# Performance work log

Measured on AMD Instinct MI355X. Metric: run time of the kernel, lower is better.

Reference implementation:

```python
import jax, jax.numpy as jnp
import numpy as np

N_GRAPHS = 50
EPS = 1e-5
N_NODES, N_EDGES, F, L, N_HEADS = 50000, 800000, 64, 3, 3


def _bn(x, gamma, beta):
    # BatchNorm1d over nodes, training-mode (biased batch statistics)
    m = x.mean(axis=0)
    v = jnp.mean((x - m) ** 2, axis=0)
    return gamma * (x - m) * jax.lax.rsqrt(v + EPS) + beta


def _pna_layer(x, src, dst, preW, preb, postW, postb, linW, linb, avg_log, avg_lin):
    N = x.shape[0]
    # pre-MLP on concatenated (target x_i, source x_j): [E, 2F] -> [E, F]
    h = jnp.concatenate([x[dst], x[src]], axis=-1) @ preW + preb
    ones = jnp.ones((h.shape[0],), h.dtype)
    cnt = jax.ops.segment_sum(ones, dst, num_segments=N)[:, None]
    has = cnt > 0
    deg = jnp.maximum(cnt, 1.0)  # PNAConv clamps degree to >= 1
    mean = jax.ops.segment_sum(h, dst, num_segments=N) / deg
    mean2 = jax.ops.segment_sum(h * h, dst, num_segments=N) / deg
    std = jnp.sqrt(jax.nn.relu(mean2 - mean * mean) + EPS)
    mn = jnp.where(has, jax.ops.segment_min(h, dst, num_segments=N), 0.0)
    mx = jnp.where(has, jax.ops.segment_max(h, dst, num_segments=N), 0.0)
    aggr = jnp.concatenate([mean, mn, mx, std], axis=-1)  # [N, 4F]
    log_deg = jnp.log(deg + 1.0)
    out = jnp.concatenate([aggr,
                           aggr * (log_deg / avg_log),   # amplification
                           aggr * (avg_log / log_deg),   # attenuation
                           aggr * (deg / avg_lin)],      # linear
                          axis=-1)                       # [N, 16F]
    out = jnp.concatenate([x, out], axis=-1) @ postW + postb  # post-MLP [N, F]
    return out @ linW + linb


def _forward(x, deg_hist, preW, preb, postW, postb, linW, linb, bn_g, bn_b,
             sharedW, sharedb, hW1, hb1, hW2, hb2, hW3, hb3, src, dst, batch):
    bins = jnp.arange(deg_hist.shape[0], dtype=deg_hist.dtype)
    tot = deg_hist.sum()
    avg_lin = (bins * deg_hist).sum() / tot
    avg_log = (jnp.log(bins + 1.0) * deg_hist).sum() / tot
    for l in range(preW.shape[0]):  # only num_conv_layers convs run (zip truncation)
        x = _pna_layer(x, src, dst, preW[l], preb[l], postW[l], postb[l],
                       linW[l], linb[l], avg_log, avg_lin)
        x = jax.nn.relu(_bn(x, bn_g[l], bn_b[l]))
    gcnt = jax.ops.segment_sum(jnp.ones((x.shape[0],), x.dtype), batch,
                               num_segments=N_GRAPHS)[:, None]
    g = jax.ops.segment_sum(x, batch, num_segments=N_GRAPHS) / jnp.maximum(gcnt, 1.0)
    g = jax.nn.relu(g @ sharedW + sharedb)  # shared MLP (num_shared=1)
    h1 = jax.nn.relu(jnp.einsum('gd,hdk->hgk', g, hW1) + hb1[:, None, :])
    h2 = jax.nn.relu(jnp.einsum('hgk,hkm->hgm', h1, hW2) + hb2[:, None, :])
    o = jnp.einsum('hgm,hmo->hgo', h2, hW3) + hb3[:, None, :]  # [H, G, 1]
    return jnp.transpose(o[..., 0])  # [G, H] == torch.cat(head outputs, dim=1)


def setup_inputs():
    key = jax.random.key(0)
    ks = jax.random.split(key, 12)

    def w(k, shape, fan_in):
        return jax.random.normal(k, shape, jnp.float32) / np.sqrt(fan_in)

    return {
        "x": jax.random.normal(ks[0], (N_NODES, F), jnp.float32),
        "edge_index": jax.random.randint(ks[1], (2, N_EDGES), 0, N_NODES),
        "batch": jnp.sort(jax.random.randint(ks[2], (N_NODES,), 0, N_GRAPHS)),
        "deg_hist": jax.random.uniform(ks[3], (33,), jnp.float32) + 0.01,
        "preW": w(ks[4], (L, 2 * F, F), 2 * F),
        "preb": jnp.zeros((L, F), jnp.float32),
        "postW": w(ks[5], (L, 17 * F, F), 17 * F),
        "postb": jnp.zeros((L, F), jnp.float32),
        "linW": w(ks[6], (L, F, F), F),
        "linb": jnp.zeros((L, F), jnp.float32),
        "bn_g": jnp.ones((L, F), jnp.float32),
        "bn_b": jnp.zeros((L, F), jnp.float32),
        "sharedW": w(ks[7], (F, F), F),
        "sharedb": jnp.zeros((F,), jnp.float32),
        "hW1": w(ks[8], (N_HEADS, F, 50), F),
        "hb1": jnp.zeros((N_HEADS, 50), jnp.float32),
        "hW2": w(ks[9], (N_HEADS, 50, 25), 50),
        "hb2": jnp.zeros((N_HEADS, 25), jnp.float32),
        "hW3": w(ks[10], (N_HEADS, 25, 1), 25),
        "hb3": jnp.zeros((N_HEADS, 1), jnp.float32),
    }


def reference(x, edge_index, batch, deg_hist, preW, preb, postW, postb,
              linW, linb, bn_g, bn_b, sharedW, sharedb,
              hW1, hb1, hW2, hb2, hW3, hb3):
    return _forward(x, deg_hist, preW, preb, postW, postb, linW, linb,
                    bn_g, bn_b, sharedW, sharedb, hW1, hb1, hW2, hb2,
                    hW3, hb3, edge_index[0], edge_index[1], batch)
```

## Files before the change

kernel.cpp:

```cpp
#include <hip/hip_runtime.h>
#include <math.h>

#define N_NODES 50000
#define N_EDGES 800000
#define NGRAPHS 50
#define NHEADS 3
#define EPS 1e-5f
#define NWIN 196
#define WSH 8

typedef _Float16 half8 __attribute__((ext_vector_type(8)));
typedef _Float16 half2v __attribute__((ext_vector_type(2)));
typedef float f32x4 __attribute__((ext_vector_type(4)));

__global__ void __launch_bounds__(256) k_zero_setup(int* cnt, float* gsum, float* gcnt,
                                                    float* part, float* partq,
                                                    const float* dh, int nbins, float* scal) {
  int gid = blockIdx.x * 256 + threadIdx.x;
  int gs = gridDim.x * 256;
  for (int i = gid; i < N_NODES; i += gs) cnt[i] = 0;
  for (int i = gid; i < NGRAPHS * 64; i += gs) gsum[i] = 0.f;
  for (int i = gid; i < NGRAPHS; i += gs) gcnt[i] = 0.f;
  for (int i = gid; i < 128 * 64; i += gs) { part[i] = 0.f; partq[i] = 0.f; }
  if (blockIdx.x == 0 && threadIdx.x < 64) {
    int t = threadIdx.x;
    float v = (t < nbins) ? dh[t] : 0.f;
    float lv = logf((float)t + 1.f) * v;
    float bv = (float)t * v;
    for (int d = 32; d > 0; d >>= 1) {
      v  += __shfl_down(v,  d, 64);
      lv += __shfl_down(lv, d, 64);
      bv += __shfl_down(bv, d, 64);
    }
    if (t == 0) { scal[0] = lv / v; scal[1] = bv / v; }
  }
}

__global__ void __launch_bounds__(256) k_hist(const int* __restrict__ dst, int* __restrict__ cnt) {
  int e = blockIdx.x * 256 + threadIdx.x;
  if (e < N_EDGES) atomicAdd(&cnt[dst[e]], 1);
}

__global__ void __launch_bounds__(256) k_scan_a(const int* __restrict__ cnt, int* __restrict__ off,
                                                int* __restrict__ blksum) {
  __shared__ int lds[256];
  int t = threadIdx.x;
  int base = blockIdx.x * 1024 + t * 4;
  int v0 = (base + 0 < N_NODES) ? cnt[base + 0] : 0;
  int v1 = (base + 1 < N_NODES) ? cnt[base + 1] : 0;
  int v2 = (base + 2 < N_NODES) ? cnt[base + 2] : 0;
  int v3 = (base + 3 < N_NODES) ? cnt[base + 3] : 0;
  int tsum = v0 + v1 + v2 + v3;
  lds[t] = tsum; __syncthreads();
  for (int d = 1; d < 256; d <<= 1) {
    int x = (t >= d) ? lds[t - d] : 0;
    __syncthreads();
    lds[t] += x;
    __syncthreads();
  }
  int run = lds[t] - tsum;
  if (base + 0 < N_NODES) off[base + 0] = run; run += v0;
  if (base + 1 < N_NODES) off[base + 1] = run; run += v1;
  if (base + 2 < N_NODES) off[base + 2] = run; run += v2;
  if (base + 3 < N_NODES) off[base + 3] = run;
  if (t == 255) blksum[blockIdx.x] = lds[255];
}

__global__ void __launch_bounds__(64) k_scan_b(const int* __restrict__ blksum, int* __restrict__ blkoff) {
  int t = threadIdx.x;
  int own = (t < 49) ? blksum[t] : 0;
  int v = own;
  for (int d = 1; d < 64; d <<= 1) {
    int u = __shfl_up(v, d, 64);
    if (t >= d) v += u;
  }
  if (t < 49) blkoff[t] = v - own;
}

__global__ void __launch_bounds__(256) k_scan_c(int* __restrict__ off, const int* __restrict__ blkoff,
                                                int* __restrict__ wincur) {
  int i = blockIdx.x * 256 + threadIdx.x;
  if (i < N_NODES) {
    int fo = off[i] + blkoff[i >> 10];
    off[i] = fo;
    if ((i & 255) == 0) wincur[i >> WSH] = fo;
  }
  if (i == 0) off[N_NODES] = N_EDGES;
}

__global__ void __launch_bounds__(256) k_part1(const int* __restrict__ src, const int* __restrict__ dst,
                                               int* __restrict__ wincur, int* __restrict__ pairS,
                                               unsigned char* __restrict__ pairDL) {
  __shared__ int hist[256];
  __shared__ int scan[256];
  __shared__ int baseg[256];
  __shared__ int place[256];
  __shared__ int sS[2048];
  __shared__ unsigned char sDL[2048];
  __shared__ unsigned char sW[2048];
  int t = threadIdx.x;
  int base = blockIdx.x * 2048;
  hist[t] = 0;
  __syncthreads();
  int d[8], s[8];
  #pragma unroll
  for (int i = 0; i < 8; ++i) {
    int e = base + t + 256 * i;
    bool val = e < N_EDGES;
    d[i] = val ? dst[e] : -1;
    s[i] = val ? src[e] : 0;
    if (val) atomicAdd(&hist[d[i] >> WSH], 1);
  }
  __syncthreads();
  int v = hist[t];
  scan[t] = v; __syncthreads();
  for (int dd = 1; dd < 256; dd <<= 1) {
    int x = (t >= dd) ? scan[t - dd] : 0;
    __syncthreads();
    scan[t] += x;
    __syncthreads();
  }
  place[t] = scan[t] - v;
  if (v > 0) baseg[t] = atomicAdd(&wincur[t], v);
  __syncthreads();
  #pragma unroll
  for (int i = 0; i < 8; ++i) {
    if (d[i] >= 0) {
      int w = d[i] >> WSH;
      int p = atomicAdd(&place[w], 1);
      sS[p] = s[i] << 6;
      sDL[p] = (unsigned char)(d[i] & 255);
      sW[p] = (unsigned char)w;
    }
  }
  __syncthreads();
  int tot = min(N_EDGES - base, 2048);
  for (int i = t; i < tot; i += 256) {
    int w = sW[i];
    int gidx = baseg[w] + (i - (scan[w] - hist[w]));
    pairS[gidx] = sS[i];
    pairDL[gidx] = sDL[i];
  }
}

__global__ void __launch_bounds__(256) k_part2(const int* __restrict__ off, const int* __restrict__ pairS,
                                               const unsigned char* __restrict__ pairDL,
                                               int* __restrict__ esrc) {
  __shared__ int curW[256];
  __shared__ int offW[257];
  __shared__ int esrcW[6144];
  int w = blockIdx.x, t = threadIdx.x;
  int n0 = w << WSH;
  offW[t] = off[min(n0 + t, N_NODES)];
  if (t == 0) offW[256] = off[min(n0 + 256, N_NODES)];
  curW[t] = 0;
  __syncthreads();
  int start = offW[0];
  int end = offW[256];
  int cnt = end - start;
  if (cnt <= 6144) {
    for (int i = t; i < cnt; i += 256) {
      int s = pairS[start + i];
      int dl = pairDL[start + i];
      int pos = offW[dl] - start + atomicAdd(&curW[dl], 1);
      esrcW[pos] = s;
    }
    __syncthreads();
    for (int i = t; i < cnt; i += 256) esrc[start + i] = esrcW[i];
  } else {
    for (int i = t; i < cnt; i += 256) {
      int s = pairS[start + i];
      int dl = pairDL[start + i];
      int pos = offW[dl] + atomicAdd(&curW[dl], 1);
      esrc[pos] = s;
    }
  }
}

__global__ void __launch_bounds__(256) k_prep(const float* __restrict__ xin, _Float16* __restrict__ xout,
                                              const float* __restrict__ preW, const float* __restrict__ postW,
                                              const float* __restrict__ linW, _Float16* __restrict__ preP,
                                              _Float16* __restrict__ postAP, _Float16* __restrict__ postBP,
                                              _Float16* __restrict__ linP) {
  int t0 = blockIdx.x * 256 + threadIdx.x;
  if (t0 < 400000) {
    const float* s = xin + (size_t)t0 * 8;
    float4 v0 = *(const float4*)s;
    float4 v1 = *(const float4*)(s + 4);
    half8 h = {(_Float16)v0.x, (_Float16)v0.y, (_Float16)v0.z, (_Float16)v0.w,
               (_Float16)v1.x, (_Float16)v1.y, (_Float16)v1.z, (_Float16)v1.w};
    *(half8*)(xout + (size_t)t0 * 8) = h;
    return;
  }
  int t = t0 - 400000;
  if (t < 24576) {
    int l = t >> 13, r = t & 8191;
    int j = r & 7, lane = (r >> 3) & 63, ctg = (r >> 9) & 7, kc = r >> 12;
    int k = kc * 32 + ((lane >> 4) << 3) + j;
    int col = ctg * 16 + (lane & 15);
    const float* W = preW + (size_t)l * 8192;
    float v = (col < 64) ? W[k * 64 + col] : W[(64 + k) * 64 + (col - 64)];
    preP[(size_t)l * 8192 + r] = (_Float16)v;
  } else if (t < 221184) {
    int q = t - 24576;
    int l = q >> 16, r = q & 65535;
    int j = r & 7, lane = (r >> 3) & 63, ct = (r >> 9) & 3, s = (r >> 11) & 3, kc = r >> 13;
    int kp = kc * 32 + ((lane >> 4) << 3) + j;
    int half = kp >> 7, sec = (kp >> 5) & 3, f = kp & 31;
    int korig = sec * 64 + half * 32 + f;
    int col = ct * 16 + (lane & 15);
    postAP[(size_t)l * 65536 + r] = (_Float16)postW[(size_t)l * 69632 + (size_t)(64 + s * 256 + korig) * 64 + col];
  } else if (t < 233472) {
    int q = t - 221184;
    int l = q >> 12, r = q & 4095;
    int j = r & 7, lane = (r >> 3) & 63, ct = (r >> 9) & 3, kc = r >> 11;
    int k = kc * 32 + ((lane >> 4) << 3) + j;
    int col = ct * 16 + (lane & 15);
    postBP[(size_t)l * 4096 + r] = (_Float16)postW[(size_t)l * 69632 + (size_t)k * 64 + col];
  } else if (t < 245760) {
    int q = t - 233472;
    int l = q >> 12, r = q & 4095;
    int j = r & 7, lane = (r >> 3) & 63, ct = (r >> 9) & 3, kc = r >> 11;
    int k = kc * 32 + ((lane >> 4) << 3) + j;
    int col = ct * 16 + (lane & 15);
    linP[(size_t)l * 4096 + r] = (_Float16)linW[(size_t)l * 4096 + (size_t)k * 64 + col];
  }
}

__global__ void __launch_bounds__(256) k_mfma_g1(const _Float16* __restrict__ yin, const float* __restrict__ bnsc,
                                                 const float* __restrict__ bnsh, int applyBN,
                                                 const _Float16* __restrict__ wp, const float* __restrict__ bias,
                                                 _Float16* __restrict__ Aout, _Float16* __restrict__ B0,
                                                 _Float16* __restrict__ B1, _Float16* __restrict__ xout) {
  int t = threadIdx.x, lane = t & 63, wave = t >> 6;
  int r0 = blockIdx.x * 64;
  int mrow = lane & 15, q8 = ((lane >> 4) << 3);
  f32x4 acc[4][2];
  #pragma unroll
  for (int rt = 0; rt < 4; ++rt) { acc[rt][0] = (f32x4)0.f; acc[rt][1] = (f32x4)0.f; }
  #pragma unroll
  for (int kc = 0; kc < 2; ++kc) {
    int k0 = kc * 32 + q8;
    half8 a[4];
    #pragma unroll
    for (int rt = 0; rt < 4; ++rt) {
      int r = min(r0 + rt * 16 + mrow, N_NODES - 1);
      a[rt] = *(const half8*)(yin + (size_t)r * 64 + k0);
    }
    if (applyBN) {
      float4 sc0 = *(const float4*)(bnsc + k0);
      float4 sc1 = *(const float4*)(bnsc + k0 + 4);
      float4 sh0 = *(const float4*)(bnsh + k0);
      float4 sh1 = *(const float4*)(bnsh + k0 + 4);
      #pragma unroll
      for (int rt = 0; rt < 4; ++rt) {
        half8 v = a[rt];
        v[0] = (_Float16)fmaxf((float)v[0] * sc0.x + sh0.x, 0.f);
        v[1] = (_Float16)fmaxf((float)v[1] * sc0.y + sh0.y, 0.f);
        v[2] = (_Float16)fmaxf((float)v[2] * sc0.z + sh0.z, 0.f);
        v[3] = (_Float16)fmaxf((float)v[3] * sc0.w + sh0.w, 0.f);
        v[4] = (_Float16)fmaxf((float)v[4] * sc1.x + sh1.x, 0.f);
        v[5] = (_Float16)fmaxf((float)v[5] * sc1.y + sh1.y, 0.f);
        v[6] = (_Float16)fmaxf((float)v[6] * sc1.z + sh1.z, 0.f);
        v[7] = (_Float16)fmaxf((float)v[7] * sc1.w + sh1.w, 0.f);
        a[rt] = v;
      }
      if (wave == 0) {
        #pragma unroll
        for (int rt = 0; rt < 4; ++rt) {
          int r = min(r0 + rt * 16 + mrow, N_NODES - 1);
          *(half8*)(xout + (size_t)r * 64 + k0) = a[rt];
        }
      }
    }
    #pragma unroll
    for (int ci = 0; ci < 2; ++ci) {
      int ctg = wave * 2 + ci;
      half8 b = *(const half8*)(wp + (size_t)((kc * 8 + ctg) * 64 + lane) * 8);
      #pragma unroll
      for (int rt = 0; rt < 4; ++rt)
        acc[rt][ci] = __builtin_amdgcn_mfma_f32_16x16x32_f16(a[rt], b, acc[rt][ci], 0, 0, 0);
    }
  }
  #pragma unroll
  for (int ci = 0; ci < 2; ++ci) {
    int col = (wave * 2 + ci) * 16 + mrow;
    float bv = (col < 64) ? bias[col] : 0.f;
    _Float16* outp;
    int stride;
    if (col < 64)      { outp = Aout + col;       stride = 64; }
    else if (col < 96) { outp = B0 + (col - 64);  stride = 32; }
    else               { outp = B1 + (col - 96);  stride = 32; }
    #pragma unroll
    for (int rt = 0; rt < 4; ++rt)
      #pragma unroll
      for (int reg = 0; reg < 4; ++reg) {
        int row = r0 + rt * 16 + ((lane >> 4) << 2) + reg;
        if (row < N_NODES) outp[(size_t)row * stride] = (_Float16)(acc[rt][ci][reg] + bv);
      }
  }
}

__global__ void __launch_bounds__(256) k_aggr(const _Float16* __restrict__ A, const _Float16* __restrict__ B0,
                                              const _Float16* __restrict__ B1, const int* __restrict__ off,
                                              const int* __restrict__ esrc, const float* __restrict__ scal,
                                              _Float16* __restrict__ aggr0, _Float16* __restrict__ aggr1,
                                              float4* __restrict__ scales) {
  int wave = threadIdx.x >> 6, lane = threadIdx.x & 63;
  int half = blockIdx.x >= 12500;
  int bb = blockIdx.x - half * 12500;
  int n = bb * 4 + wave;
  if (n >= N_NODES) return;
  int lh4 = lane & 15, eg = lane >> 4;
  half2v c2 = *(const half2v*)(A + (size_t)n * 64 + half * 32 + lh4 * 2);
  float c0 = (float)c2[0], c1 = (float)c2[1];
  int e0 = __builtin_amdgcn_readfirstlane(off[n]);
  int e1 = __builtin_amdgcn_readfirstlane(off[n + 1]);
  int deg = e1 - e0;
  const char* Bb = (const char*)(half ? B1 : B0);
  int lo4 = lh4 * 4;
  float s0 = 0.f, s1 = 0.f, q0 = 0.f, q1 = 0.f;
  float mn0 = 3.4e38f, mn1 = 3.4e38f, mx0 = -3.4e38f, mx1 = -3.4e38f;
  int e = e0;
  for (; e + 7 < e1; e += 8) {
    int ra = esrc[e + eg];
    int rb = esrc[e + 4 + eg];
    half2v ba = *(const half2v*)(Bb + ra + lo4);
    half2v bb2 = *(const half2v*)(Bb + rb + lo4);
    float a0 = (float)ba[0], a1 = (float)ba[1];
    float b0 = (float)bb2[0], b1 = (float)bb2[1];
    s0 += a0 + b0; s1 += a1 + b1;
    q0 += a0 * a0; q0 += b0 * b0; q1 += a1 * a1; q1 += b1 * b1;
    mn0 = fminf(mn0, fminf(a0, b0)); mn1 = fminf(mn1, fminf(a1, b1));
    mx0 = fmaxf(mx0, fmaxf(a0, b0)); mx1 = fmaxf(mx1, fmaxf(a1, b1));
  }
  for (; e < e1; e += 4) {
    if (e + eg < e1) {
      int r = esrc[e + eg];
      half2v bv = *(const half2v*)(Bb + r + lo4);
      float a0 = (float)bv[0], a1 = (float)bv[1];
      s0 += a0; s1 += a1;
      q0 += a0 * a0; q1 += a1 * a1;
      mn0 = fminf(mn0, a0); mn1 = fminf(mn1, a1);
      mx0 = fmaxf(mx0, a0); mx1 = fmaxf(mx1, a1);
    }
  }
  s0 += __shfl_xor(s0, 16, 64); s0 += __shfl_xor(s0, 32, 64);
  s1 += __shfl_xor(s1, 16, 64); s1 += __shfl_xor(s1, 32, 64);
  q0 += __shfl_xor(q0, 16, 64); q0 += __shfl_xor(q0, 32, 64);
  q1 += __shfl_xor(q1, 16, 64); q1 += __shfl_xor(q1, 32, 64);
  mn0 = fminf(mn0, __shfl_xor(mn0, 16, 64)); mn0 = fminf(mn0, __shfl_xor(mn0, 32, 64));
  mn1 = fminf(mn1, __shfl_xor(mn1, 16, 64)); mn1 = fminf(mn1, __shfl_xor(mn1, 32, 64));
  mx0 = fmaxf(mx0, __shfl_xor(mx0, 16, 64)); mx0 = fmaxf(mx0, __shfl_xor(mx0, 32, 64));
  mx1 = fmaxf(mx1, __shfl_xor(mx1, 16, 64)); mx1 = fmaxf(mx1, __shfl_xor(mx1, 32, 64));
  if (eg == 0) {
    _Float16* arow = (half ? aggr1 : aggr0) + (size_t)n * 128;
    half2v w;
    if (deg == 0) {
      w[0] = (_Float16)0.f; w[1] = (_Float16)0.f;
      *(half2v*)(arow + lh4 * 2) = w;
      *(half2v*)(arow + 32 + lh4 * 2) = w;
      *(half2v*)(arow + 64 + lh4 * 2) = w;
      w[0] = (_Float16)sqrtf(EPS); w[1] = w[0];
      *(half2v*)(arow + 96 + lh4 * 2) = w;
    } else {
      float inv = 1.f / (float)deg;
      float mb0 = s0 * inv, mb1 = s1 * inv;
      float v0 = fmaxf(q0 * inv - mb0 * mb0, 0.f);
      float v1 = fmaxf(q1 * inv - mb1 * mb1, 0.f);
      w[0] = (_Float16)(c0 + mb0); w[1] = (_Float16)(c1 + mb1);
      *(half2v*)(arow + lh4 * 2) = w;
      w[0] = (_Float16)(c0 + mn0); w[1] = (_Float16)(c1 + mn1);
      *(half2v*)(arow + 32 + lh4 * 2) = w;
      w[0] = (_Float16)(c0 + mx0); w[1] = (_Float16)(c1 + mx1);
      *(half2v*)(arow + 64 + lh4 * 2) = w;
      w[0] = (_Float16)sqrtf(v0 + EPS); w[1] = (_Float16)sqrtf(v1 + EPS);
      *(half2v*)(arow + 96 + lh4 * 2) = w;
    }
    if (half == 0 && lane == 0) {
      float degf = fmaxf((float)deg, 1.f);
      float ld = logf(degf + 1.f);
      float al = scal[0], av = scal[1];
      scales[n] = make_float4(ld / al, al / ld, degf / av, 0.f);
    }
  }
}

__global__ void __launch_bounds__(256) k_mfma_g23(const _Float16* __restrict__ aggr0, const _Float16* __restrict__ aggr1,
                                                  const _Float16* __restrict__ x16,
                                                  const _Float16* __restrict__ wpA, const _Float16* __restrict__ wpB,
                                                  const float* __restrict__ postb, const float4* __restrict__ scales,
                                                  const _Float16* __restrict__ linP, const float* __restrict__ linb,
                                                  _Float16* __restrict__ y16,
                                                  float* __restrict__ part, float* __restrict__ partq) {
  __shared__ _Float16 yS[64][72];
  int t = threadIdx.x, lane = t & 63, ct = t >> 6;
  int r0 = blockIdx.x * 64;
  int mrow = lane & 15, q8 = ((lane >> 4) << 3);
  f32x4 acc[4][4];
  #pragma unroll
  for (int rt = 0; rt < 4; ++rt)
    #pragma unroll
    for (int s = 0; s < 4; ++s) acc[rt][s] = (f32x4)0.f;
  #pragma unroll 2
  for (int kc = 0; kc < 8; ++kc) {
    const _Float16* ab = (kc < 4) ? aggr0 : aggr1;
    int ko = (kc & 3) * 32 + q8;
    half8 a[4];
    #pragma unroll
    for (int rt = 0; rt < 4; ++rt) {
      int r = min(r0 + rt * 16 + mrow, N_NODES - 1);
      a[rt] = *(const half8*)(ab + (size_t)r * 128 + ko);
    }
    #pragma unroll
    for (int s = 0; s < 4; ++s) {
      half8 b = *(const half8*)(wpA + (size_t)((((kc * 4 + s) * 4 + ct) * 64) + lane) * 8);
      #pragma unroll
      for (int rt = 0; rt < 4; ++rt)
        acc[rt][s] = __builtin_amdgcn_mfma_f32_16x16x32_f16(a[rt], b, acc[rt][s], 0, 0, 0);
    }
  }
  #pragma unroll
  for (int kc = 0; kc < 2; ++kc) {
    half8 a[4];
    #pragma unroll
    for (int rt = 0; rt < 4; ++rt) {
      int r = min(r0 + rt * 16 + mrow, N_NODES - 1);
      a[rt] = *(const half8*)(x16 + (size_t)r * 64 + kc * 32 + q8);
    }
    half8 b = *(const half8*)(wpB + (size_t)(((kc * 4 + ct) * 64) + lane) * 8);
    #pragma unroll
    for (int rt = 0; rt < 4; ++rt)
      acc[rt][0] = __builtin_amdgcn_mfma_f32_16x16x32_f16(a[rt], b, acc[rt][0], 0, 0, 0);
  }
  int col = ct * 16 + mrow;
  float pb = postb[col];
  #pragma unroll
  for (int rt = 0; rt < 4; ++rt)
    #pragma unroll
    for (int reg = 0; reg < 4; ++reg) {
      int rr = rt * 16 + ((lane >> 4) << 2) + reg;
      int row = min(r0 + rr, N_NODES - 1);
      float4 sc = scales[row];
      float v = acc[rt][0][reg] + sc.x * acc[rt][1][reg] + sc.y * acc[rt][2][reg] + sc.z * acc[rt][3][reg] + pb;
      yS[rr][col] = (_Float16)v;
    }
  __syncthreads();
  f32x4 acc2[4];
  #pragma unroll
  for (int rt = 0; rt < 4; ++rt) acc2[rt] = (f32x4)0.f;
  #pragma unroll
  for (int kc = 0; kc < 2; ++kc) {
    half8 a[4];
    #pragma unroll
    for (int rt = 0; rt < 4; ++rt)
      a[rt] = *(const half8*)(&yS[rt * 16 + mrow][kc * 32 + q8]);
    half8 b = *(const half8*)(linP + (size_t)(((kc * 4 + ct) * 64) + lane) * 8);
    #pragma unroll
    for (int rt = 0; rt < 4; ++rt)
      acc2[rt] = __builtin_amdgcn_mfma_f32_16x16x32_f16(a[rt], b, acc2[rt], 0, 0, 0);
  }
  float bv = linb[col];
  float s = 0.f, q = 0.f;
  #pragma unroll
  for (int rt = 0; rt < 4; ++rt)
    #pragma unroll
    for (int reg = 0; reg < 4; ++reg) {
      int row = r0 + rt * 16 + ((lane >> 4) << 2) + reg;
      if (row < N_NODES) {
        float v = acc2[rt][reg] + bv;
        y16[(size_t)row * 64 + col] = (_Float16)v;
        s += v; q += v * v;
      }
    }
  int slot = (blockIdx.x & 127) * 64 + col;
  atomicAdd(&part[slot], s);
  atomicAdd(&partq[slot], q);
}

__global__ void __launch_bounds__(256) k_bnfinal(float* __restrict__ part, float* __restrict__ partq,
                                                 const float* __restrict__ g, const float* __restrict__ b,
                                                 float* __restrict__ scale, float* __restrict__ shift) {
  __shared__ float ls[256], lq[256];
  int t = threadIdx.x, col = t & 63, qtr = t >> 6;
  float s = 0.f, q = 0.f;
  for (int i = 0; i < 32; ++i) {
    int slot = qtr * 32 + i;
    s += part[slot * 64 + col];
    q += partq[slot * 64 + col];
  }
  ls[t] = s; lq[t] = q; __syncthreads();
  if (t < 64) {
    s = ls[t] + ls[64 + t] + ls[128 + t] + ls[192 + t];
    q = lq[t] + lq[64 + t] + lq[128 + t] + lq[192 + t];
    float m = s / (float)N_NODES;
    float v = fmaxf(q / (float)N_NODES - m * m, 0.f);
    float sc = g[t] * rsqrtf(v + EPS);
    scale[t] = sc;
    shift[t] = b[t] - m * sc;
  }
  __syncthreads();
  for (int i = t; i < 128 * 64; i += 256) { part[i] = 0.f; partq[i] = 0.f; }
}

__global__ void __launch_bounds__(256) k_pool(const _Float16* __restrict__ y16, const float* __restrict__ bnsc,
                                              const float* __restrict__ bnsh, const int* __restrict__ batch,
                                              float* __restrict__ gsum, float* __restrict__ gcnt) {
  int t = threadIdx.x, col = t & 63, rl = t >> 6;
  float sc = bnsc[col], sh = bnsh[col];
  int rbeg = blockIdx.x * 64 + rl * 16;
  int rend = min(rbeg + 16, N_NODES);
  int curg = -1, cr = 0;
  float acc = 0.f;
  for (int r = rbeg; r < rend; ++r) {
    int g = batch[r];
    if (g != curg) {
      if (curg >= 0) {
        atomicAdd(&gsum[curg * 64 + col], acc);
        if (col == 0) atomicAdd(&gcnt[curg], (float)cr);
      }
      curg = g; acc = 0.f; cr = 0;
    }
    acc += fmaxf((float)y16[(size_t)r * 64 + col] * sc + sh, 0.f); cr++;
  }
  if (curg >= 0) {
    atomicAdd(&gsum[curg * 64 + col], acc);
    if (col == 0) atomicAdd(&gcnt[curg], (float)cr);
  }
}

__global__ void __launch_bounds__(64) k_sharedheads(const float* __restrict__ gsum, const float* __restrict__ gcnt,
                                                    const float* __restrict__ W, const float* __restrict__ b,
                                                    const float* __restrict__ hW1, const float* __restrict__ hb1,
                                                    const float* __restrict__ hW2, const float* __restrict__ hb2,
                                                    const float* __restrict__ hW3, const float* __restrict__ hb3,
                                                    float* __restrict__ out) {
  __shared__ float gm[64], gv[64], h1[50], h2[25];
  int bid = blockIdx.x;
  int g = bid / NHEADS, h = bid % NHEADS;
  int t = threadIdx.x;
  float cv = fmaxf(gcnt[g], 1.f);
  gm[t] = gsum[g * 64 + t] / cv;
  __syncthreads();
  float s0 = b[t];
  for (int k = 0; k < 64; ++k) s0 += gm[k] * W[k * 64 + t];
  gv[t] = fmaxf(s0, 0.f);
  __syncthreads();
  if (t < 50) {
    float s = hb1[h * 50 + t];
    for (int k = 0; k < 64; ++k) s += gv[k] * hW1[h * 3200 + k * 50 + t];
    h1[t] = fmaxf(s, 0.f);
  }
  __syncthreads();
  if (t < 25) {
    float s = hb2[h * 25 + t];
    for (int k = 0; k < 50; ++k) s += h1[k] * hW2[h * 1250 + k * 25 + t];
    h2[t] = fmaxf(s, 0.f);
  }
  __syncthreads();
  if (t == 0) {
    float s = hb3[h];
    for (int k = 0; k < 25; ++k) s += h2[k] * hW3[h * 25 + k];
    out[g * NHEADS + h] = s;
  }
}

extern "C" void kernel_launch(void* const* d_in, const int* in_sizes, int n_in,
                              void* d_out, int out_size, void* d_ws, size_t ws_size,
                              hipStream_t stream) {
  const float* x0    = (const float*)d_in[0];
  const int*   eidx  = (const int*)d_in[1];
  const int*   batch = (const int*)d_in[2];
  const float* dh    = (const float*)d_in[3];
  const float* preW  = (const float*)d_in[4];
  const float* preb  = (const float*)d_in[5];
  const float* postW = (const float*)d_in[6];
  const float* postb = (const float*)d_in[7];
  const float* linW  = (const float*)d_in[8];
  const float* linb  = (const float*)d_in[9];
  const float* bng   = (const float*)d_in[10];
  const float* bnb   = (const float*)d_in[11];
  const float* shW   = (const float*)d_in[12];
  const float* shb   = (const float*)d_in[13];
  const float* hW1   = (const float*)d_in[14];
  const float* hb1   = (const float*)d_in[15];
  const float* hW2   = (const float*)d_in[16];
  const float* hb2   = (const float*)d_in[17];
  const float* hW3   = (const float*)d_in[18];
  const float* hb3   = (const float*)d_in[19];
  float* out = (float*)d_out;

  char* ws = (char*)d_ws;
  size_t o = 0;
  auto alloc = [&](size_t bytes) {
    char* p = ws + o;
    o = (o + bytes + 255) & ~(size_t)255;
    return p;
  };
  float* scal   = (float*)alloc(8 * 4);
  int* off      = (int*)alloc((N_NODES + 1) * 4);
  int* cnt      = (int*)alloc(N_NODES * 4);
  int* esrc     = (int*)alloc(N_EDGES * 4);
  int* pairS    = (int*)alloc(N_EDGES * 4);
  unsigned char* pairDL = (unsigned char*)alloc(N_EDGES);
  int* wincur   = (int*)alloc(NWIN * 4);
  int* blks     = (int*)alloc(64 * 4);
  int* blko     = (int*)alloc(64 * 4);
  _Float16* A16    = (_Float16*)alloc((size_t)N_NODES * 64 * 2 + 256 * 16);
  _Float16* B0     = (_Float16*)alloc((size_t)N_NODES * 32 * 2 + 256 * 16);
  _Float16* B1     = (_Float16*)alloc((size_t)N_NODES * 32 * 2 + 256 * 16);
  _Float16* aggr0  = (_Float16*)alloc((size_t)N_NODES * 128 * 2 + 256 * 16);
  _Float16* aggr1  = (_Float16*)alloc((size_t)N_NODES * 128 * 2 + 256 * 16);
  _Float16* x16a   = (_Float16*)alloc((size_t)N_NODES * 64 * 2 + 256 * 16);
  _Float16* xbuf   = (_Float16*)alloc((size_t)N_NODES * 64 * 2 + 256 * 16);
  _Float16* y16    = (_Float16*)alloc((size_t)N_NODES * 64 * 2 + 256 * 16);
  float4* scales = (float4*)alloc((size_t)N_NODES * 16);
  _Float16* preP   = (_Float16*)alloc(3 * 8192 * 2);
  _Float16* postAP = (_Float16*)alloc((size_t)3 * 65536 * 2);
  _Float16* postBP = (_Float16*)alloc(3 * 4096 * 2);
  _Float16* linP   = (_Float16*)alloc(3 * 4096 * 2);
  float* part   = (float*)alloc(128 * 64 * 4);
  float* partq  = (float*)alloc(128 * 64 * 4);
  float* bnsc   = (float*)alloc(64 * 4);
  float* bnsh   = (float*)alloc(64 * 4);
  float* gsum   = (float*)alloc(NGRAPHS * 64 * 4);
  float* gcnt   = (float*)alloc(NGRAPHS * 4);

  const int* srcv = eidx;
  const int* dstv = eidx + N_EDGES;

  k_zero_setup<<<256, 256, 0, stream>>>(cnt, gsum, gcnt, part, partq, dh, in_sizes[3], scal);
  k_hist<<<(N_EDGES + 255) / 256, 256, 0, stream>>>(dstv, cnt);
  k_scan_a<<<49, 256, 0, stream>>>(cnt, off, blks);
  k_scan_b<<<1, 64, 0, stream>>>(blks, blko);
  k_scan_c<<<196, 256, 0, stream>>>(off, blko, wincur);
  k_part1<<<(N_EDGES + 2047) / 2048, 256, 0, stream>>>(srcv, dstv, wincur, pairS, pairDL);
  k_part2<<<NWIN, 256, 0, stream>>>(off, pairS, pairDL, esrc);
  k_prep<<<(400000 + 245760 + 255) / 256, 256, 0, stream>>>(x0, x16a, preW, postW, linW,
                                                            preP, postAP, postBP, linP);

  for (int l = 0; l < 3; ++l) {
    const _Float16* g1in = (l == 0) ? x16a : y16;
    const _Float16* xc   = (l == 0) ? x16a : xbuf;
    k_mfma_g1<<<782, 256, 0, stream>>>(g1in, bnsc, bnsh, (l > 0) ? 1 : 0,
                                       preP + (size_t)l * 8192, preb + l * 64, A16, B0, B1, xbuf);
    k_aggr<<<25000, 256, 0, stream>>>(A16, B0, B1, off, esrc, scal, aggr0, aggr1, scales);
    k_mfma_g23<<<782, 256, 0, stream>>>(aggr0, aggr1, xc, postAP + (size_t)l * 65536,
                                        postBP + (size_t)l * 4096, postb + l * 64, scales,
                                        linP + (size_t)l * 4096, linb + l * 64, y16, part, partq);
    k_bnfinal<<<1, 256, 0, stream>>>(part, partq, bng + l * 64, bnb + l * 64, bnsc, bnsh);
  }
  k_pool<<<782, 256, 0, stream>>>(y16, bnsc, bnsh, batch, gsum, gcnt);
  k_sharedheads<<<NGRAPHS * NHEADS, 64, 0, stream>>>(gsum, gcnt, shW, shb,
                                                     hW1, hb1, hW2, hb2, hW3, hb3, out);
}
```

Before: 499.2 us.

## Aggregate in packed fp16, interleave block halves, use nontemporal loads/stores

```diff
diff --git a/kernel.cpp b/kernel.cpp
--- a/kernel.cpp
+++ b/kernel.cpp
@@ -12,6 +12,11 @@
 typedef _Float16 half8 __attribute__((ext_vector_type(8)));
 typedef _Float16 half2v __attribute__((ext_vector_type(2)));
 typedef float f32x4 __attribute__((ext_vector_type(4)));
+
+__device__ inline half2v h2_shfl_xor(half2v v, int m) {
+  int xi = __shfl_xor(*(int*)&v, m, 64);
+  return *(half2v*)&xi;
+}
 
 __global__ void __launch_bounds__(256) k_zero_setup(int* cnt, float* gsum, float* gcnt,
                                                     float* part, float* partq,
@@ -307,75 +312,73 @@
                                               _Float16* __restrict__ aggr0, _Float16* __restrict__ aggr1,
                                               float4* __restrict__ scales) {
   int wave = threadIdx.x >> 6, lane = threadIdx.x & 63;
-  int half = blockIdx.x >= 12500;
-  int bb = blockIdx.x - half * 12500;
-  int n = bb * 4 + wave;
-  if (n >= N_NODES) return;
+  int b = blockIdx.x;
+  int half = (b >> 2) & 1;
+  int idx = (b >> 3) * 4 + (b & 3);
+  int n = idx * 4 + wave;
   int lh4 = lane & 15, eg = lane >> 4;
   half2v c2 = *(const half2v*)(A + (size_t)n * 64 + half * 32 + lh4 * 2);
-  float c0 = (float)c2[0], c1 = (float)c2[1];
   int e0 = __builtin_amdgcn_readfirstlane(off[n]);
   int e1 = __builtin_amdgcn_readfirstlane(off[n + 1]);
   int deg = e1 - e0;
   const char* Bb = (const char*)(half ? B1 : B0);
   int lo4 = lh4 * 4;
-  float s0 = 0.f, s1 = 0.f, q0 = 0.f, q1 = 0.f;
-  float mn0 = 3.4e38f, mn1 = 3.4e38f, mx0 = -3.4e38f, mx1 = -3.4e38f;
+  const _Float16 HMAX = (_Float16)65504.f;
+  half2v s2 = {(_Float16)0.f, (_Float16)0.f};
+  half2v q2 = s2;
+  half2v mn2 = {HMAX, HMAX};
+  half2v mx2 = {-HMAX, -HMAX};
   int e = e0;
   for (; e + 7 < e1; e += 8) {
-    int ra = esrc[e + eg];
-    int rb = esrc[e + 4 + eg];
+    int ra = __builtin_nontemporal_load(esrc + e + eg);
+    int rb = __builtin_nontemporal_load(esrc + e + 4 + eg);
     half2v ba = *(const half2v*)(Bb + ra + lo4);
-    half2v bb2 = *(const half2v*)(Bb + rb + lo4);
-    float a0 = (float)ba[0], a1 = (float)ba[1];
-    float b0 = (float)bb2[0], b1 = (float)bb2[1];
-    s0 += a0 + b0; s1 += a1 + b1;
-    q0 += a0 * a0; q0 += b0 * b0; q1 += a1 * a1; q1 += b1 * b1;
-    mn0 = fminf(mn0, fminf(a0, b0)); mn1 = fminf(mn1, fminf(a1, b1));
-    mx0 = fmaxf(mx0, fmaxf(a0, b0)); mx1 = fmaxf(mx1, fmaxf(a1, b1));
+    half2v bb = *(const half2v*)(Bb + rb + lo4);
+    s2 += ba; s2 += bb;
+    q2 += ba * ba; q2 += bb * bb;
+    mn2 = __builtin_elementwise_min(mn2, __builtin_elementwise_min(ba, bb));
+    mx2 = __builtin_elementwise_max(mx2, __builtin_elementwise_max(ba, bb));
   }
   for (; e < e1; e += 4) {
     if (e + eg < e1) {
-      int r = esrc[e + eg];
+      int r = __builtin_nontemporal_load(esrc + e + eg);
       half2v bv = *(const half2v*)(Bb + r + lo4);
-      float a0 = (float)bv[0], a1 = (float)bv[1];
-      s0 += a0; s1 += a1;
-      q0 += a0 * a0; q1 += a1 * a1;
-      mn0 = fminf(mn0, a0); mn1 = fminf(mn1, a1);
-      mx0 = fmaxf(mx0, a0); mx1 = fmaxf(mx1, a1);
-    }
-  }
-  s0 += __shfl_xor(s0, 16, 64); s0 += __shfl_xor(s0, 32, 64);
-  s1 += __shfl_xor(s1, 16, 64); s1 += __shfl_xor(s1, 32, 64);
-  q0 += __shfl_xor(q0, 16, 64); q0 += __shfl_xor(q0, 32, 64);
-  q1 += __shfl_xor(q1, 16, 64); q1 += __shfl_xor(q1, 32, 64);
-  mn0 = fminf(mn0, __shfl_xor(mn0, 16, 64)); mn0 = fminf(mn0, __shfl_xor(mn0, 32, 64));
-  mn1 = fminf(mn1, __shfl_xor(mn1, 16, 64)); mn1 = fminf(mn1, __shfl_xor(mn1, 32, 64));
-  mx0 = fmaxf(mx0, __shfl_xor(mx0, 16, 64)); mx0 = fmaxf(mx0, __shfl_xor(mx0, 32, 64));
-  mx1 = fmaxf(mx1, __shfl_xor(mx1, 16, 64)); mx1 = fmaxf(mx1, __shfl_xor(mx1, 32, 64));
+      s2 += bv;
+      q2 += bv * bv;
+      mn2 = __builtin_elementwise_min(mn2, bv);
+      mx2 = __builtin_elementwise_max(mx2, bv);
+    }
+  }
+  s2 += h2_shfl_xor(s2, 16); s2 += h2_shfl_xor(s2, 32);
+  q2 += h2_shfl_xor(q2, 16); q2 += h2_shfl_xor(q2, 32);
+  mn2 = __builtin_elementwise_min(mn2, h2_shfl_xor(mn2, 16));
+  mn2 = __builtin_elementwise_min(mn2, h2_shfl_xor(mn2, 32));
+  mx2 = __builtin_elementwise_max(mx2, h2_shfl_xor(mx2, 16));
+  mx2 = __builtin_elementwise_max(mx2, h2_shfl_xor(mx2, 32));
   if (eg == 0) {
     _Float16* arow = (half ? aggr1 : aggr0) + (size_t)n * 128;
     half2v w;
     if (deg == 0) {
       w[0] = (_Float16)0.f; w[1] = (_Float16)0.f;
-      *(half2v*)(arow + lh4 * 2) = w;
-      *(half2v*)(arow + 32 + lh4 * 2) = w;
-      *(half2v*)(arow + 64 + lh4 * 2) = w;
+      __builtin_nontemporal_store(w, (half2v*)(arow + lh4 * 2));
+      __builtin_nontemporal_store(w, (half2v*)(arow + 32 + lh4 * 2));
+      __builtin_nontemporal_store(w, (half2v*)(arow + 64 + lh4 * 2));
       w[0] = (_Float16)sqrtf(EPS); w[1] = w[0];
-      *(half2v*)(arow + 96 + lh4 * 2) = w;
+      __builtin_nontemporal_store(w, (half2v*)(arow + 96 + lh4 * 2));
     } else {
+      float c0 = (float)c2[0], c1 = (float)c2[1];
       float inv = 1.f / (float)deg;
-      float mb0 = s0 * inv, mb1 = s1 * inv;
-      float v0 = fmaxf(q0 * inv - mb0 * mb0, 0.f);
-      float v1 = fmaxf(q1 * inv - mb1 * mb1, 0.f);
+      float mb0 = (float)s2[0] * inv, mb1 = (float)s2[1] * inv;
+      float v0 = fmaxf((float)q2[0] * inv - mb0 * mb0, 0.f);
+      float v1 = fmaxf((float)q2[1] * inv - mb1 * mb1, 0.f);
       w[0] = (_Float16)(c0 + mb0); w[1] = (_Float16)(c1 + mb1);
-      *(half2v*)(arow + lh4 * 2) = w;
-      w[0] = (_Float16)(c0 + mn0); w[1] = (_Float16)(c1 + mn1);
-      *(half2v*)(arow + 32 + lh4 * 2) = w;
-      w[0] = (_Float16)(c0 + mx0); w[1] = (_Float16)(c1 + mx1);
-      *(half2v*)(arow + 64 + lh4 * 2) = w;
+      __builtin_nontemporal_store(w, (half2v*)(arow + lh4 * 2));
+      w[0] = (_Float16)(c0 + (float)mn2[0]); w[1] = (_Float16)(c1 + (float)mn2[1]);
+      __builtin_nontemporal_store(w, (half2v*)(arow + 32 + lh4 * 2));
+      w[0] = (_Float16)(c0 + (float)mx2[0]); w[1] = (_Float16)(c1 + (float)mx2[1]);
+      __builtin_nontemporal_store(w, (half2v*)(arow + 64 + lh4 * 2));
       w[0] = (_Float16)sqrtf(v0 + EPS); w[1] = (_Float16)sqrtf(v1 + EPS);
-      *(half2v*)(arow + 96 + lh4 * 2) = w;
+      __builtin_nontemporal_store(w, (half2v*)(arow + 96 + lh4 * 2));
     }
     if (half == 0 && lane == 0) {
       float degf = fmaxf((float)deg, 1.f);
@@ -410,7 +413,7 @@
     #pragma unroll
     for (int rt = 0; rt < 4; ++rt) {
       int r = min(r0 + rt * 16 + mrow, N_NODES - 1);
-      a[rt] = *(const half8*)(ab + (size_t)r * 128 + ko);
+      a[rt] = __builtin_nontemporal_load((const half8*)(ab + (size_t)r * 128 + ko));
     }
     #pragma unroll
     for (int s = 0; s < 4; ++s) {
```

Measured after the change: 535.7 us. 7.3% more time.
